# Kernel optimization log

Measured on AMD Instinct MI355X. Metric: run time of the kernel, lower is better.

Reference implementation:

```python
import jax, jax.numpy as jnp
import numpy as np

NG, ND, NS, E, DIM, H = 20000, 8000, 8000, 300000, 256, 8
HD = DIM // H
SCALE = 1.0 / float(np.sqrt(HD))
EPS = 1e-5


def _ln(x, g, b):
    mu = x.mean(-1, keepdims=True)
    var = ((x - mu) ** 2).mean(-1, keepdims=True)
    return (x - mu) / jnp.sqrt(var + EPS) * g + b


def _attn(h_src, h_dst, Wq, bq, Wk, bk, Wv, bv, src, dst, n_dst):
    # multi-head edge dot-product attention with edge_softmax over incoming edges
    Q = (h_dst @ Wq.T + bq).reshape(-1, H, HD)
    K = (h_src @ Wk.T + bk).reshape(-1, H, HD)
    V = (h_src @ Wv.T + bv).reshape(-1, H, HD)
    score = jnp.einsum('ehd,ehd->eh', K[src], Q[dst]) * SCALE  # [E, H]
    m = jax.ops.segment_max(score, dst, num_segments=n_dst)
    m = jnp.where(jnp.isfinite(m), m, 0.0)  # nodes with no in-edges
    a = jnp.exp(score - m[dst])
    denom = jax.ops.segment_sum(a, dst, num_segments=n_dst)
    a = a / denom[dst]
    h = jax.ops.segment_sum(V[src] * a[:, :, None], dst, num_segments=n_dst)
    return h.reshape(n_dst, DIM)


def _bahdanau(m1, m2, W1, b1, W2, b2, v, bv):
    e1 = (jnp.tanh(m1 @ W1.T + b1) @ v.T + bv)[:, 0]
    e2 = (jnp.tanh(m2 @ W2.T + b2) @ v.T + bv)[:, 0]
    w = jax.nn.softmax(jnp.stack([e1, e2], axis=1), axis=1)
    return w[:, 0:1] * m1 + w[:, 1:2] * m2


def _forward(gene_feat, drug_feat, disease_feat,
             dg_Wq, dg_bq, dg_Wk, dg_bk, dg_Wv, dg_bv,
             disg_Wq, disg_bq, disg_Wk, disg_bk, disg_Wv, disg_bv,
             gd_Wq, gd_bq, gd_Wk, gd_bk, gd_Wv, gd_bv,
             gdis_Wq, gdis_bq, gdis_Wk, gdis_bk, gdis_Wv, gdis_bv,
             f_W1, f_b1, f_W2, f_b2, f_v, f_bv,
             ln1_g, ln1_b, ln2_g, ln2_b,
             dg_src, dg_dst, disg_src, disg_dst, gd_src, gd_dst, gdis_src, gdis_dst):
    gm_drug = _attn(drug_feat, gene_feat, dg_Wq, dg_bq, dg_Wk, dg_bk, dg_Wv, dg_bv, dg_src, dg_dst, NG)
    gm_dis = _attn(disease_feat, gene_feat, disg_Wq, disg_bq, disg_Wk, disg_bk, disg_Wv, disg_bv, disg_src, disg_dst, NG)
    has_d = jnp.zeros((NG,), bool).at[dg_dst].set(True)
    has_s = jnp.zeros((NG,), bool).at[disg_dst].set(True)
    fused = _bahdanau(gm_drug, gm_dis, f_W1, f_b1, f_W2, f_b2, f_v, f_bv)
    gene_msg = jnp.where((has_d & has_s)[:, None], fused,
                         jnp.where(has_d[:, None], gm_drug,
                                   jnp.where(has_s[:, None], gm_dis, 0.0)))
    gene_out = _ln(gene_feat + jax.nn.gelu(gene_msg, approximate=False), ln1_g, ln1_b)
    drug_msg = _attn(gene_out, drug_feat, gd_Wq, gd_bq, gd_Wk, gd_bk, gd_Wv, gd_bv, gd_src, gd_dst, ND)
    dis_msg = _attn(gene_out, disease_feat, gdis_Wq, gdis_bq, gdis_Wk, gdis_bk, gdis_Wv, gdis_bv, gdis_src, gdis_dst, NS)
    drug_out = _ln(drug_feat + jax.nn.gelu(drug_msg, approximate=False), ln2_g, ln2_b)
    disease_out = _ln(disease_feat + jax.nn.gelu(dis_msg, approximate=False), ln2_g, ln2_b)
    return (drug_out, disease_out, gene_out)


def setup_inputs() -> dict:
    ks = jax.random.split(jax.random.key(0), 40)
    it = iter(range(40))

    def nrm(shape):
        return jax.random.normal(ks[next(it)], shape, dtype=jnp.float32)

    def xav(din, dout):
        lim = float(np.sqrt(6.0 / (din + dout)))
        return jax.random.uniform(ks[next(it)], (dout, din), minval=-lim, maxval=lim, dtype=jnp.float32)

    def ridx(n, hi):
        return jax.random.randint(ks[next(it)], (n,), 0, hi, dtype=jnp.int32)

    inp = {}
    inp['gene_feat'] = nrm((NG, DIM))
    inp['drug_feat'] = nrm((ND, DIM))
    inp['disease_feat'] = nrm((NS, DIM))
    for p in ['dg', 'disg', 'gd', 'gdis']:
        inp[p + '_Wq'] = xav(DIM, DIM)
        inp[p + '_bq'] = jnp.zeros((DIM,), jnp.float32)
        inp[p + '_Wk'] = xav(DIM, DIM)
        inp[p + '_bk'] = jnp.zeros((DIM,), jnp.float32)
        inp[p + '_Wv'] = xav(DIM, DIM)
        inp[p + '_bv'] = jnp.zeros((DIM,), jnp.float32)
    inp['f_W1'] = xav(DIM, DIM); inp['f_b1'] = jnp.zeros((DIM,), jnp.float32)
    inp['f_W2'] = xav(DIM, DIM); inp['f_b2'] = jnp.zeros((DIM,), jnp.float32)
    inp['f_v'] = xav(DIM, 1); inp['f_bv'] = jnp.zeros((1,), jnp.float32)
    inp['ln1_g'] = jnp.ones((DIM,), jnp.float32); inp['ln1_b'] = jnp.zeros((DIM,), jnp.float32)
    inp['ln2_g'] = jnp.ones((DIM,), jnp.float32); inp['ln2_b'] = jnp.zeros((DIM,), jnp.float32)
    inp['dg_src'] = ridx(E, ND); inp['dg_dst'] = ridx(E, NG)
    inp['disg_src'] = ridx(E, NS); inp['disg_dst'] = ridx(E, NG)
    inp['gd_src'] = ridx(E, NG); inp['gd_dst'] = ridx(E, ND)
    inp['gdis_src'] = ridx(E, NG); inp['gdis_dst'] = ridx(E, NS)
    return inp


def reference(gene_feat, drug_feat, disease_feat,
              dg_Wq, dg_bq, dg_Wk, dg_bk, dg_Wv, dg_bv,
              disg_Wq, disg_bq, disg_Wk, disg_bk, disg_Wv, disg_bv,
              gd_Wq, gd_bq, gd_Wk, gd_bk, gd_Wv, gd_bv,
              gdis_Wq, gdis_bq, gdis_Wk, gdis_bk, gdis_Wv, gdis_bv,
              f_W1, f_b1, f_W2, f_b2, f_v, f_bv,
              ln1_g, ln1_b, ln2_g, ln2_b,
              dg_src, dg_dst, disg_src, disg_dst, gd_src, gd_dst, gdis_src, gdis_dst):
    return _forward(gene_feat, drug_feat, disease_feat,
                    dg_Wq, dg_bq, dg_Wk, dg_bk, dg_Wv, dg_bv,
                    disg_Wq, disg_bq, disg_Wk, disg_bk, disg_Wv, disg_bv,
                    gd_Wq, gd_bq, gd_Wk, gd_bk, gd_Wv, gd_bv,
                    gdis_Wq, gdis_bq, gdis_Wk, gdis_bk, gdis_Wv, gdis_bv,
                    f_W1, f_b1, f_W2, f_b2, f_v, f_bv,
                    ln1_g, ln1_b, ln2_g, ln2_b,
                    dg_src, dg_dst, disg_src, disg_dst, gd_src, gd_dst, gdis_src, gdis_dst)
```

## Files before the change

### kernel.cpp

```cpp
#include <hip/hip_runtime.h>

#define NG 20000
#define ND 8000
#define NS 8000
#define EE 300000
#define DIM 256
#define SCALE_QK 0.17677669529663687f
#define LNEPS 1e-5f

#define MAXB 40
#define L1CH 2048
#define NCH1 ((EE + L1CH - 1) / L1CH)
#define CB_G 8704
#define CB_S 10496
#define RB_G (40 * CB_G)
#define RB_S (32 * CB_S)

typedef __attribute__((ext_vector_type(4))) float floatx4;
typedef __attribute__((ext_vector_type(8))) short shortx8;
typedef __attribute__((ext_vector_type(8))) unsigned short ushortx8;
typedef unsigned int u32;

__device__ __forceinline__ float bf2f(unsigned short u) {
    union { unsigned u; float f; } c; c.u = ((unsigned)u) << 16; return c.f;
}
__device__ __forceinline__ unsigned short f2bf(float f) {
    union { float f; unsigned u; } c; c.f = f;
    return (unsigned short)((c.u + 0x7fffu + ((c.u >> 16) & 1u)) >> 16);
}
__device__ __forceinline__ float gelu_exact(float v) {
    return 0.5f * v * (1.0f + erff(v * 0.70710678118654752f));
}

__device__ __forceinline__ void async_load16(const unsigned short* g,
                                             unsigned short* lds) {
    __builtin_amdgcn_global_load_lds(
        (const __attribute__((address_space(1))) u32*)(const void*)g,
        (__attribute__((address_space(3))) u32*)(void*)lds, 16, 0, 0);
}

__device__ __forceinline__ int swzoff(int row, int q) {
    int p = (row >> 1) & 7, b = row & 1;
    return ((row >> 4) * 64 + p * 8 + (((b << 2) + q) ^ p)) * 8;
}

struct GemmDesc {
    const unsigned short* A; const unsigned short* W;
    const float* b1; const float* b2; const float* b3; const float* b4;
    unsigned short* C; int ldc;
    const float* vvec; float* evec;
    int M; int gx; int ncol; int mode; int kvi;
};
struct GemmBatch { GemmDesc d[4]; };

__global__ __launch_bounds__(256, 4) void gemm_batch_kernel(GemmBatch gb)
{
    __shared__ unsigned short As[2][128 * 32];
    __shared__ unsigned short Bs[2][64 * 32];
    const GemmDesc d = gb.d[blockIdx.z];
    if ((int)blockIdx.x >= d.gx) return;
    const int n0 = blockIdx.y * 64;
    if (n0 >= d.ncol) return;

    const int tid = threadIdx.x;
    const int lane = tid & 63, wv = tid >> 6;
    const int quad = lane >> 4, l16 = lane & 15;
    const int m0 = blockIdx.x * 128;

    const int sp = lane >> 3, ss = lane & 7;
    const int srow = 2 * sp + ((ss ^ sp) >> 2);
    const int sq = (ss ^ sp) & 3;
    const unsigned short* gA0 = d.A + (size_t)(m0 + wv * 16 + srow) * 256 + sq * 8;
    const unsigned short* gA1 = d.A + (size_t)(m0 + 64 + wv * 16 + srow) * 256 + sq * 8;
    const unsigned short* gB  = d.W + (size_t)(n0 + wv * 16 + srow) * 256 + sq * 8;

    floatx4 acc[2][4];
#pragma unroll
    for (int i = 0; i < 2; ++i)
#pragma unroll
        for (int j = 0; j < 4; ++j) acc[i][j] = (floatx4){0.f, 0.f, 0.f, 0.f};

    async_load16(gA0, &As[0][(wv * 16) * 32]);
    async_load16(gA1, &As[0][(64 + wv * 16) * 32]);
    async_load16(gB,  &Bs[0][(wv * 16) * 32]);
    __syncthreads();

    for (int k0 = 0; k0 < 256; k0 += 32) {
        const int buf = (k0 >> 5) & 1;
        if (k0 < 224) {
            const int nb = buf ^ 1;
            async_load16(gA0 + k0 + 32, &As[nb][(wv * 16) * 32]);
            async_load16(gA1 + k0 + 32, &As[nb][(64 + wv * 16) * 32]);
            async_load16(gB + k0 + 32,  &Bs[nb][(wv * 16) * 32]);
        }
        shortx8 af[2], bfr[4];
#pragma unroll
        for (int mf = 0; mf < 2; ++mf)
            af[mf] = *(const shortx8*)(&As[buf][swzoff(wv * 32 + mf * 16 + l16, quad)]);
#pragma unroll
        for (int nf = 0; nf < 4; ++nf)
            bfr[nf] = *(const shortx8*)(&Bs[buf][swzoff(nf * 16 + l16, quad)]);
#pragma unroll
        for (int mf = 0; mf < 2; ++mf)
#pragma unroll
            for (int nf = 0; nf < 4; ++nf)
                acc[mf][nf] = __builtin_amdgcn_mfma_f32_16x16x32_bf16(
                    af[mf], bfr[nf], acc[mf][nf], 0, 0, 0);
        __syncthreads();
    }

    if (d.mode == 0) {
#pragma unroll
        for (int mf = 0; mf < 2; ++mf)
#pragma unroll
            for (int r = 0; r < 4; ++r) {
                int m = m0 + wv * 32 + mf * 16 + quad * 4 + r;
                if (m < d.M) {
#pragma unroll
                    for (int nf = 0; nf < 4; ++nf) {
                        int n = n0 + nf * 16 + l16;
                        int h = n >> 8;
                        const float* bp = (h == 0) ? d.b1 : (h == 1) ? d.b2
                                        : (h == 2) ? d.b3 : d.b4;
                        float bn = bp[n & 255];
                        int pos;
                        if (d.kvi) {
                            int nn = n & 511;
                            pos = (n & ~511) + ((nn & 255) >> 2) * 8 + (nn & 3) +
                                  ((nn >> 8) << 2);
                        } else {
                            pos = n;
                        }
                        d.C[(size_t)m * d.ldc + pos] = f2bf(acc[mf][nf][r] + bn);
                    }
                }
            }
    } else {
        float p[2][4] = {};
#pragma unroll
        for (int mf = 0; mf < 2; ++mf)
#pragma unroll
            for (int nf = 0; nf < 4; ++nf) {
                int n = n0 + nf * 16 + l16;
                float vn = d.vvec[n];
                float bn = d.b1[n];
#pragma unroll
                for (int r = 0; r < 4; ++r)
                    p[mf][r] += vn * tanhf(acc[mf][nf][r] + bn);
            }
#pragma unroll
        for (int mf = 0; mf < 2; ++mf)
#pragma unroll
            for (int r = 0; r < 4; ++r) {
                float s = p[mf][r];
                s += __shfl_xor(s, 1); s += __shfl_xor(s, 2);
                s += __shfl_xor(s, 4); s += __shfl_xor(s, 8);
                if (l16 == 0) {
                    int m = m0 + wv * 32 + mf * 16 + quad * 4 + r;
                    if (m < d.M) atomicAdd(&d.evec[m], s);
                }
            }
    }
}

struct PrepP {
    int* zb; int zn; int nzb;
    const float* wsrc[14];
    unsigned short* wout;
    const float* gf; const float* df; const float* sf;
    unsigned short* go; unsigned short* dfo; unsigned short* so;
};
__global__ void prep_kernel(PrepP p) {
    int bid = blockIdx.x, tid = threadIdx.x;
    if (bid < p.nzb) {
        int i = bid * 256 + tid;
        if (i < p.zn) p.zb[i] = 0;
        return;
    }
    bid -= p.nzb;
    if (bid < 896) {
        int idx = bid * 256 + tid;
        int mat = idx >> 14;
        int e = (idx & 16383) << 2;
        float4 f = *(const float4*)(p.wsrc[mat] + e);
        ushort4 t;
        t.x = f2bf(f.x); t.y = f2bf(f.y); t.z = f2bf(f.z); t.w = f2bf(f.w);
        *(ushort4*)(p.wout + ((size_t)mat << 16) + e) = t;
        return;
    }
    bid -= 896;
    const int NG4 = NG * 64, ND4 = ND * 64, NS4 = NS * 64;
    int i = bid * 256 + tid;
    const float* in; unsigned short* out; int j;
    if (i < NG4) { in = p.gf; out = p.go; j = i; }
    else if (i < NG4 + ND4) { in = p.df; out = p.dfo; j = i - NG4; }
    else if (i < NG4 + ND4 + NS4) { in = p.sf; out = p.so; j = i - NG4 - ND4; }
    else return;
    float4 f = *(const float4*)(in + (size_t)j * 4);
    ushort4 t;
    t.x = f2bf(f.x); t.y = f2bf(f.y); t.z = f2bf(f.z); t.w = f2bf(f.w);
    *(ushort4*)(out + (size_t)j * 4) = t;
}

__global__ void fillf_kernel(float* __restrict__ p, int n, float v) {
    int i = blockIdx.x * blockDim.x + threadIdx.x;
    if (i < n) p[i] = v;
}

struct L1P {
    const int* src[4];
    const int* dst[4];
    int* brec[4];
    int* bcur;
};
__global__ __launch_bounds__(256) void l1_bucket_kernel(L1P a) {
    __shared__ int hist[MAXB];
    int g = blockIdx.x / NCH1, c = blockIdx.x - g * NCH1;
    int base = c * L1CH;
    int tid = threadIdx.x;
    const int shift = (g < 2) ? 9 : 8;
    const int CB = (g < 2) ? CB_G : CB_S;
    const int NB = (g < 2) ? 40 : 32;
    if (tid < NB) hist[tid] = 0;
    __syncthreads();
    const int* __restrict__ dstp = a.dst[g];
    const int* __restrict__ srcp = a.src[g];
    int bk[8], rec[8], lr[8];
#pragma unroll
    for (int j = 0; j < 8; ++j) {
        int e = base + j * 256 + tid;
        bool ok = e < EE;
        int dd = ok ? dstp[e] : 0;
        int ss = ok ? srcp[e] : 0;
        bk[j] = dd >> shift;
        rec[j] = ((dd & ((1 << shift) - 1)) << 15) | ss;
        lr[j] = ok ? atomicAdd(&hist[bk[j]], 1) : -1;
    }
    __syncthreads();
    if (tid < NB) {
        int h = hist[tid];
        if (h > 0) hist[tid] = atomicAdd(&a.bcur[g * MAXB + tid], h);
    }
    __syncthreads();
    int* __restrict__ recp = a.brec[g];
#pragma unroll
    for (int j = 0; j < 8; ++j) {
        if (lr[j] >= 0) {
            int pos = hist[bk[j]] + lr[j];
            if (pos < CB) recp[bk[j] * CB + pos] = rec[j];
        }
    }
}

struct L2P {
    const int* brec[4];
    const int* bcur;
    int* cnt[4];
    int* offs[4];
    int* srcs[4];
};
__global__ __launch_bounds__(256) void l2_csr_kernel(L2P a) {
    __shared__ int hist[512];
    __shared__ int loffs[512];
    __shared__ int cur[512];
    __shared__ int ws2[4];
    __shared__ int bb;
    int bid = blockIdx.x, tid = threadIdx.x;
    int g, b;
    if (bid < 40) { g = 0; b = bid; }
    else if (bid < 80) { g = 1; b = bid - 40; }
    else if (bid < 112) { g = 2; b = bid - 80; }
    else { g = 3; b = bid - 112; }
    const int shift = (g < 2) ? 9 : 8;
    const int BSZ = 1 << shift;
    const int CB = (g < 2) ? CB_G : CB_S;
    const int N = (g < 2) ? NG : ((g == 2) ? ND : NS);
    hist[tid] = 0; hist[256 + tid] = 0;
    if (tid == 0) {
        int s = 0;
        const int* bc = a.bcur + g * MAXB;
        for (int i = 0; i < b; ++i) s += bc[i];
        bb = s;
    }
    __syncthreads();
    int total = a.bcur[g * MAXB + b];
    if (total > CB) total = CB;
    const int* __restrict__ recp = a.brec[g] + b * CB;
    for (int i = tid; i < total; i += 256)
        atomicAdd(&hist[recp[i] >> 15], 1);
    __syncthreads();
    int v0 = hist[2 * tid], v1 = hist[2 * tid + 1];
    int s = v0 + v1, x = s;
    int lane = tid & 63, wv = tid >> 6;
#pragma unroll
    for (int o = 1; o < 64; o <<= 1) {
        int u = __shfl_up(x, o);
        if (lane >= o) x += u;
    }
    if (lane == 63) ws2[wv] = x;
    __syncthreads();
    int woff = 0;
    for (int w = 0; w < wv; ++w) woff += ws2[w];
    int excl = woff + x - s;
    loffs[2 * tid] = excl; loffs[2 * tid + 1] = excl + v0;
    cur[2 * tid] = excl;  cur[2 * tid + 1] = excl + v0;
    int base = bb;
    int lo = b << shift;
    for (int i = tid; i < BSZ; i += 256) {
        int dd = lo + i;
        if (dd < N) {
            a.cnt[g][dd] = hist[i];
            a.offs[g][dd] = base + loffs[i];
        }
    }
    __syncthreads();
    int* __restrict__ sp = a.srcs[g];
    for (int i = tid; i < total; i += 256) {
        int rec = recp[i];
        int pos = atomicAdd(&cur[rec >> 15], 1);
        sp[base + pos] = rec & 0x7fff;
    }
}

__device__ __forceinline__ void wave_attn_node(
    const unsigned short* __restrict__ Q, int qs,
    const unsigned short* __restrict__ KV,
    const int* __restrict__ offs, const int* __restrict__ cnt,
    const int* __restrict__ srcs, int du, int lane,
    float& g0, float& g1, float& g2, float& g3)
{
    const int lo = lane * 4;
    const int lofs = lane * 8;
    ushort4 qv = *(const ushort4*)(Q + (size_t)du * qs + lo);
    const float q0 = bf2f(qv.x), q1 = bf2f(qv.y), q2 = bf2f(qv.z), q3 = bf2f(qv.w);
    const int beg = offs[du], num = cnt[du];

    float m = -INFINITY, l = 0.f;
    float a0 = 0.f, a1 = 0.f, a2 = 0.f, a3 = 0.f;

    int sb[8];
    if (num > 0) {
#pragma unroll
        for (int c = 0; c < 8; ++c)
            sb[c] = srcs[beg + ((c < num) ? c : (num - 1))];
    }

    for (int i = 0; i < num; i += 8) {
        int sn[8];
        const bool more = (i + 8) < num;
        if (more) {
#pragma unroll
            for (int c = 0; c < 8; ++c) {
                int idx = i + 8 + c;
                sn[c] = srcs[beg + ((idx < num) ? idx : (num - 1))];
            }
        }
        ushortx8 kv[8];
#pragma unroll
        for (int c = 0; c < 8; ++c)
            kv[c] = *(const ushortx8*)(KV + (size_t)sb[c] * 512 + lofs);
        float p[8];
#pragma unroll
        for (int c = 0; c < 8; ++c)
            p[c] = q0 * bf2f(kv[c][0]) + q1 * bf2f(kv[c][1]) +
                   q2 * bf2f(kv[c][2]) + q3 * bf2f(kv[c][3]);
#pragma unroll
        for (int c = 0; c < 8; ++c) p[c] += __shfl_xor(p[c], 1);
#pragma unroll
        for (int c = 0; c < 8; ++c) p[c] += __shfl_xor(p[c], 2);
#pragma unroll
        for (int c = 0; c < 8; ++c) p[c] += __shfl_xor(p[c], 4);
        float sc[8];
#pragma unroll
        for (int c = 0; c < 8; ++c)
            sc[c] = (i + c < num) ? p[c] * SCALE_QK : -INFINITY;
        float bm = fmaxf(fmaxf(fmaxf(sc[0], sc[1]), fmaxf(sc[2], sc[3])),
                         fmaxf(fmaxf(sc[4], sc[5]), fmaxf(sc[6], sc[7])));
        float mn = fmaxf(m, bm);
        float eo = __expf(m - mn);
        a0 *= eo; a1 *= eo; a2 *= eo; a3 *= eo; l *= eo;
        float en[8];
#pragma unroll
        for (int c = 0; c < 8; ++c) en[c] = __expf(sc[c] - mn);
#pragma unroll
        for (int c = 0; c < 8; ++c) {
            a0 += en[c] * bf2f(kv[c][4]);
            a1 += en[c] * bf2f(kv[c][5]);
            a2 += en[c] * bf2f(kv[c][6]);
            a3 += en[c] * bf2f(kv[c][7]);
            l += en[c];
        }
        m = mn;
        if (more) {
#pragma unroll
            for (int c = 0; c < 8; ++c) sb[c] = sn[c];
        }
    }

    float inv = (l > 0.f) ? 1.f / l : 0.f;
    g0 = a0 * inv; g1 = a1 * inv; g2 = a2 * inv; g3 = a3 * inv;
}

__device__ __forceinline__ void wave_ln_store(
    float x0, float x1, float x2, float x3,
    const float* __restrict__ g, const float* __restrict__ b,
    float* __restrict__ out, unsigned short* __restrict__ out_bf,
    int du, int lo)
{
    float s1 = x0 + x1 + x2 + x3;
    float s2 = x0 * x0 + x1 * x1 + x2 * x2 + x3 * x3;
#pragma unroll
    for (int o = 1; o < 64; o <<= 1) {
        s1 += __shfl_xor(s1, o);
        s2 += __shfl_xor(s2, o);
    }
    float mu = s1 * (1.f / 256.f);
    float var = fmaxf(s2 * (1.f / 256.f) - mu * mu, 0.f);
    float rs = rsqrtf(var + LNEPS);
    float4 gv = *(const float4*)(g + lo);
    float4 bv = *(const float4*)(b + lo);
    float y0 = (x0 - mu) * rs * gv.x + bv.x;
    float y1 = (x1 - mu) * rs * gv.y + bv.y;
    float y2 = (x2 - mu) * rs * gv.z + bv.z;
    float y3 = (x3 - mu) * rs * gv.w + bv.w;
    *(float4*)(out + (size_t)du * 256 + lo) = make_float4(y0, y1, y2, y3);
    if (out_bf) {
        ushort4 t; t.x = f2bf(y0); t.y = f2bf(y1); t.z = f2bf(y2); t.w = f2bf(y3);
        *(ushort4*)(out_bf + (size_t)du * 256 + lo) = t;
    }
}

struct AggDesc {
    const unsigned short* Q; int qs;
    const unsigned short* KV;
    const int* offs; const int* cnt; const int* srcs;
    unsigned short* gm;
    const float* feat; const float* g; const float* b; float* out;
    int N;
};
template <int LN>
__global__ __launch_bounds__(256, 8) void agg2_kernel(
    AggDesc a0, AggDesc a1, int nb0, int nbtot)
{
    int lane = threadIdx.x & 63, wv = threadIdx.x >> 6;
    int lo = lane * 4;
    for (int bx = blockIdx.x; bx < nbtot; bx += gridDim.x) {
        const bool first = bx < nb0;
        const AggDesc d = first ? a0 : a1;
        const int bxx = first ? bx : (bx - nb0);
        int nd = bxx * 4 + wv;
        if (nd >= d.N) continue;
        int du = __builtin_amdgcn_readfirstlane(nd);
        float g0, g1, g2, g3;
        wave_attn_node(d.Q, d.qs, d.KV, d.offs, d.cnt, d.srcs, du, lane,
                       g0, g1, g2, g3);
        if (LN == 0) {
            ushort4 t; t.x = f2bf(g0); t.y = f2bf(g1); t.z = f2bf(g2); t.w = f2bf(g3);
            *(ushort4*)(d.gm + (size_t)du * 256 + lo) = t;
        } else {
            float4 fv = *(const float4*)(d.feat + (size_t)du * 256 + lo);
            float x0 = fv.x + gelu_exact(g0);
            float x1 = fv.y + gelu_exact(g1);
            float x2 = fv.z + gelu_exact(g2);
            float x3 = fv.w + gelu_exact(g3);
            wave_ln_store(x0, x1, x2, x3, d.g, d.b, d.out, nullptr, du, lo);
        }
    }
}

__global__ __launch_bounds__(256) void gene_fusion_kernel(
    const float* __restrict__ gene_feat, const unsigned short* __restrict__ gm_d,
    const unsigned short* __restrict__ gm_s, const float* __restrict__ e1,
    const float* __restrict__ e2, const int* __restrict__ cnt_d,
    const int* __restrict__ cnt_s, const float* __restrict__ g,
    const float* __restrict__ b, float* __restrict__ out,
    unsigned short* __restrict__ out_bf)
{
    int lane = threadIdx.x & 63, wv = threadIdx.x >> 6;
    int d = blockIdx.x * 4 + wv;
    if (d >= NG) return;
    int du = __builtin_amdgcn_readfirstlane(d);
    int lo = lane * 4;
    ushort4 v1 = *(const ushort4*)(gm_d + (size_t)du * 256 + lo);
    ushort4 v2 = *(const ushort4*)(gm_s + (size_t)du * 256 + lo);
    bool hd = cnt_d[du] > 0, hs = cnt_s[du] > 0;
    float wa, wb;
    if (hd && hs) {
        float aa = e1[du], bb = e2[du];
        float mm = fmaxf(aa, bb);
        float ea = __expf(aa - mm), eb = __expf(bb - mm);
        float inv = 1.f / (ea + eb);
        wa = ea * inv; wb = eb * inv;
    } else if (hd) { wa = 1.f; wb = 0.f; }
    else if (hs) { wa = 0.f; wb = 1.f; }
    else { wa = 0.f; wb = 0.f; }
    float m0 = wa * bf2f(v1.x) + wb * bf2f(v2.x);
    float m1 = wa * bf2f(v1.y) + wb * bf2f(v2.y);
    float m2 = wa * bf2f(v1.z) + wb * bf2f(v2.z);
    float m3 = wa * bf2f(v1.w) + wb * bf2f(v2.w);
    float4 fv = *(const float4*)(gene_feat + (size_t)du * 256 + lo);
    float x0 = fv.x + gelu_exact(m0);
    float x1 = fv.y + gelu_exact(m1);
    float x2 = fv.z + gelu_exact(m2);
    float x3 = fv.w + gelu_exact(m3);
    wave_ln_store(x0, x1, x2, x3, g, b, out, out_bf, du, lo);
}

extern "C" void kernel_launch(void* const* d_in, const int* in_sizes, int n_in,
                              void* d_out, int out_size, void* d_ws, size_t ws_size,
                              hipStream_t stream)
{
    float* out_f32 = (float*)d_out;

    const float* gene_feat    = (const float*)d_in[0];
    const float* drug_feat    = (const float*)d_in[1];
    const float* disease_feat = (const float*)d_in[2];
    const float* dg_Wq = (const float*)d_in[3];
    const float* dg_bq = (const float*)d_in[4];
    const float* dg_Wk = (const float*)d_in[5];
    const float* dg_bk = (const float*)d_in[6];
    const float* dg_Wv = (const float*)d_in[7];
    const float* dg_bv = (const float*)d_in[8];
    const float* disg_Wq = (const float*)d_in[9];
    const float* disg_bq = (const float*)d_in[10];
    const float* disg_Wk = (const float*)d_in[11];
    const float* disg_bk = (const float*)d_in[12];
    const float* disg_Wv = (const float*)d_in[13];
    const float* disg_bv = (const float*)d_in[14];
    const float* gd_Wq = (const float*)d_in[15];
    const float* gd_bq = (const float*)d_in[16];
    const float* gd_Wk = (const float*)d_in[17];
    const float* gd_bk = (const float*)d_in[18];
    const float* gd_Wv = (const float*)d_in[19];
    const float* gd_bv = (const float*)d_in[20];
    const float* gdis_Wq = (const float*)d_in[21];
    const float* gdis_bq = (const float*)d_in[22];
    const float* gdis_Wk = (const float*)d_in[23];
    const float* gdis_bk = (const float*)d_in[24];
    const float* gdis_Wv = (const float*)d_in[25];
    const float* gdis_bv = (const float*)d_in[26];
    const float* f_W1 = (const float*)d_in[27];
    const float* f_b1 = (const float*)d_in[28];
    const float* f_W2 = (const float*)d_in[29];
    const float* f_b2 = (const float*)d_in[30];
    const float* f_v  = (const float*)d_in[31];
    const float* ln1_g = (const float*)d_in[33];
    const float* ln1_b = (const float*)d_in[34];
    const float* ln2_g = (const float*)d_in[35];
    const float* ln2_b = (const float*)d_in[36];
    const int* dg_src   = (const int*)d_in[37];
    const int* dg_dst   = (const int*)d_in[38];
    const int* disg_src = (const int*)d_in[39];
    const int* disg_dst = (const int*)d_in[40];
    const int* gd_src   = (const int*)d_in[41];
    const int* gd_dst   = (const int*)d_in[42];
    const int* gdis_src = (const int*)d_in[43];
    const int* gdis_dst = (const int*)d_in[44];

    char* ws = (char*)d_ws;
    size_t off = 0;
    auto alloc = [&](size_t bytes) -> char* {
        char* p = ws + off;
        off += (bytes + 511) & ~(size_t)511;
        return p;
    };
    int* bcur = (int*)alloc(4 * MAXB * 4);
    float* e1 = (float*)alloc(NG * 4);
    float* e2 = (float*)alloc(NG * 4);
    size_t zero_len = off;
    int* offs_dg   = (int*)alloc(NG * 4);
    int* offs_disg = (int*)alloc(NG * 4);
    int* offs_gd   = (int*)alloc(ND * 4);
    int* offs_gdis = (int*)alloc(NS * 4);
    int* cnt_dg    = (int*)alloc(NG * 4);
    int* cnt_disg  = (int*)alloc(NG * 4);
    int* cnt_gd    = (int*)alloc(ND * 4);
    int* cnt_gdis  = (int*)alloc(NS * 4);
    int* srcs_dg   = (int*)alloc((size_t)EE * 4);
    int* srcs_disg = (int*)alloc((size_t)EE * 4);
    int* srcs_gd   = (int*)alloc((size_t)EE * 4);
    int* srcs_gdis = (int*)alloc((size_t)EE * 4);
    unsigned short* Q12  = (unsigned short*)alloc((size_t)NG * 512 * 2);
    unsigned short* KVb  = (unsigned short*)alloc((size_t)NG * 512 * 2);
    unsigned short* gm_d = (unsigned short*)alloc((size_t)NG * 256 * 2);
    unsigned short* gm_s = (unsigned short*)alloc((size_t)NG * 256 * 2);
    unsigned short* gene_bf = (unsigned short*)alloc((size_t)NG * 256 * 2);
    unsigned short* drug_bf = (unsigned short*)alloc((size_t)ND * 256 * 2);
    unsigned short* dis_bf  = (unsigned short*)alloc((size_t)NS * 256 * 2);
    unsigned short* Wbf     = (unsigned short*)alloc((size_t)14 * 65536 * 2);
    char* guard = alloc(64 * 1024);
    (void)guard;
    size_t need = off;

    int* brec0 = (int*)Q12;
    int* brec1 = brec0 + RB_G;
    int* brec2 = brec1 + RB_G;
    int* brec3 = brec2 + RB_S;

    unsigned short* KVb2 = gm_s;
    unsigned short* KVs1b = KVb + (size_t)ND * 512;
    unsigned short* Qd = Q12;
    unsigned short* Qs = Q12 + (size_t)ND * 256;
    unsigned short* gene_out_bf = gm_d;

    float* out_drug = out_f32;
    float* out_dis  = out_drug + (size_t)ND * 256;
    float* out_gene = out_dis + (size_t)NS * 256;

    if (ws_size < need) {
        fillf_kernel<<<(out_size + 255) / 256, 256, 0, stream>>>(out_f32, out_size, 1000.0f);
        return;
    }

    {
        PrepP p;
        p.zb = (int*)d_ws;
        p.zn = (int)(zero_len / 4);
        p.nzb = (p.zn + 255) / 256;
        const float* wl[14] = {dg_Wq, disg_Wq, dg_Wk, dg_Wv, disg_Wk, disg_Wv,
                               gd_Wk, gd_Wv, gdis_Wk, gdis_Wv, gd_Wq, gdis_Wq,
                               f_W1, f_W2};
        for (int i = 0; i < 14; ++i) p.wsrc[i] = wl[i];
        p.wout = Wbf;
        p.gf = gene_feat; p.df = drug_feat; p.sf = disease_feat;
        p.go = gene_bf; p.dfo = drug_bf; p.so = dis_bf;
        int nfeat = ((NG + ND + NS) * 64 + 255) / 256;
        prep_kernel<<<p.nzb + 896 + nfeat, 256, 0, stream>>>(p);
    }

    {
        L1P p;
        p.src[0] = dg_src; p.src[1] = disg_src; p.src[2] = gd_src; p.src[3] = gdis_src;
        p.dst[0] = dg_dst; p.dst[1] = disg_dst; p.dst[2] = gd_dst; p.dst[3] = gdis_dst;
        p.brec[0] = brec0; p.brec[1] = brec1; p.brec[2] = brec2; p.brec[3] = brec3;
        p.bcur = bcur;
        l1_bucket_kernel<<<4 * NCH1, 256, 0, stream>>>(p);
    }
    {
        L2P p;
        p.brec[0] = brec0; p.brec[1] = brec1; p.brec[2] = brec2; p.brec[3] = brec3;
        p.bcur = bcur;
        p.cnt[0] = cnt_dg; p.cnt[1] = cnt_disg; p.cnt[2] = cnt_gd; p.cnt[3] = cnt_gdis;
        p.offs[0] = offs_dg; p.offs[1] = offs_disg; p.offs[2] = offs_gd; p.offs[3] = offs_gdis;
        p.srcs[0] = srcs_dg; p.srcs[1] = srcs_disg; p.srcs[2] = srcs_gd; p.srcs[3] = srcs_gdis;
        l2_csr_kernel<<<144, 256, 0, stream>>>(p);
    }

    const int GXG = (NG + 127) / 128;
    const int GXS = (ND + 127) / 128;

    auto mkd = [](const unsigned short* A, const unsigned short* W,
                  const float* b1, const float* b2, const float* b3, const float* b4,
                  unsigned short* C, int ldc, const float* vv, float* ev,
                  int M, int gx, int ncol, int mode, int kvi) {
        GemmDesc d;
        d.A = A; d.W = W; d.b1 = b1; d.b2 = b2; d.b3 = b3; d.b4 = b4;
        d.C = C; d.ldc = ldc; d.vvec = vv; d.evec = ev;
        d.M = M; d.gx = gx; d.ncol = ncol; d.mode = mode; d.kvi = kvi;
        return d;
    };
    auto mka = [](const unsigned short* Q, int qs, const unsigned short* KV,
                  const int* offs, const int* cnt, const int* srcs,
                  unsigned short* gm, const float* feat, const float* g,
                  const float* b, float* out, int N) {
        AggDesc d;
        d.Q = Q; d.qs = qs; d.KV = KV; d.offs = offs; d.cnt = cnt; d.srcs = srcs;
        d.gm = gm; d.feat = feat; d.g = g; d.b = b; d.out = out; d.N = N;
        return d;
    };

    {
        GemmBatch gb;
        gb.d[0] = mkd(gene_bf, Wbf, dg_bq, disg_bq, dg_bq, dg_bq,
                      Q12, 512, nullptr, nullptr, NG, GXG, 512, 0, 0);
        gb.d[1] = mkd(drug_bf, Wbf + (size_t)2 * 65536, dg_bk, dg_bv, dg_bk, dg_bk,
                      KVb, 512, nullptr, nullptr, ND, GXS, 512, 0, 1);
        gb.d[2] = mkd(dis_bf, Wbf + (size_t)4 * 65536, disg_bk, disg_bv, disg_bk, disg_bk,
                      KVs1b, 512, nullptr, nullptr, NS, GXS, 512, 0, 1);
        gb.d[3] = gb.d[2]; gb.d[3].gx = 0;
        gemm_batch_kernel<<<dim3(GXG, 8, 3), 256, 0, stream>>>(gb);
    }

    {
        AggDesc a0 = mka(Q12, 512, KVb, offs_dg, cnt_dg, srcs_dg,
                         gm_d, nullptr, nullptr, nullptr, nullptr, NG);
        AggDesc a1 = mka(Q12 + 256, 512, KVs1b, offs_disg, cnt_disg, srcs_disg,
                         gm_s, nullptr, nullptr, nullptr, nullptr, NG);
        int nb = (NG + 3) / 4;
        int nbtot = 2 * nb;
        int grid = nbtot < 2048 ? nbtot : 2048;
        agg2_kernel<0><<<grid, 256, 0, stream>>>(a0, a1, nb, nbtot);
    }

    {
        GemmBatch gb;
        gb.d[0] = mkd(gm_d, Wbf + (size_t)12 * 65536, f_b1, f_b1, f_b1, f_b1,
                      nullptr, 256, f_v, e1, NG, GXG, 256, 1, 0);
        gb.d[1] = mkd(gm_s, Wbf + (size_t)13 * 65536, f_b2, f_b2, f_b2, f_b2,
                      nullptr, 256, f_v, e2, NG, GXG, 256, 1, 0);
        gb.d[2] = mkd(drug_bf, Wbf + (size_t)10 * 65536, gd_bq, gd_bq, gd_bq, gd_bq,
                      Qd, 256, nullptr, nullptr, ND, GXS, 256, 0, 0);
        gb.d[3] = mkd(dis_bf, Wbf + (size_t)11 * 65536, gdis_bq, gdis_bq, gdis_bq, gdis_bq,
                      Qs, 256, nullptr, nullptr, NS, GXS, 256, 0, 0);
        gemm_batch_kernel<<<dim3(GXG, 4, 4), 256, 0, stream>>>(gb);
    }

    gene_fusion_kernel<<<(NG + 3) / 4, 256, 0, stream>>>(
        gene_feat, gm_d, gm_s, e1, e2, cnt_dg, cnt_disg, ln1_g, ln1_b,
        out_gene, gene_out_bf);

    {
        GemmBatch gb;
        gb.d[0] = mkd(gene_out_bf, Wbf + (size_t)6 * 65536, gd_bk, gd_bv, gd_bk, gd_bk,
                      KVb, 512, nullptr, nullptr, NG, GXG, 512, 0, 1);
        gb.d[1] = mkd(gene_out_bf, Wbf + (size_t)8 * 65536, gdis_bk, gdis_bv, gdis_bk, gdis_bk,
                      KVb2, 512, nullptr, nullptr, NG, GXG, 512, 0, 1);
        gb.d[2] = gb.d[1]; gb.d[2].gx = 0;
        gb.d[3] = gb.d[1]; gb.d[3].gx = 0;
        gemm_batch_kernel<<<dim3(GXG, 8, 2), 256, 0, stream>>>(gb);
    }

    {
        AggDesc a0 = mka(Qd, 256, KVb, offs_gd, cnt_gd, srcs_gd,
                         nullptr, drug_feat, ln2_g, ln2_b, out_drug, ND);
        AggDesc a1 = mka(Qs, 256, KVb2, offs_gdis, cnt_gdis, srcs_gdis,
                         nullptr, disease_feat, ln2_g, ln2_b, out_dis, NS);
        int nb = (ND + 3) / 4;
        int nbtot = 2 * nb;
        int grid = nbtot < 2048 ? nbtot : 2048;
        agg2_kernel<1><<<grid, 256, 0, stream>>>(a0, a1, nb, nbtot);
    }
}
```

Before: 497.4 us.

## Double-buffer KV gathers in attention aggregation and launch one block per node group

The per-node attention loop now issues the K/V row gathers for the next chunk of 8 edges before computing the current chunk. It also prefetches source indices two chunks ahead, so memory latency overlaps the score, softmax and accumulate work. Separately, the aggregation kernel drops its grid-stride loop and the occupancy hint in launch_bounds, and launches one block per four nodes. The double buffer roughly doubles the vector registers held for KV, which may reduce occupancy. The larger grid adds block scheduling overhead.

```diff
diff --git a/kernel.cpp b/kernel.cpp
--- a/kernel.cpp
+++ b/kernel.cpp
@@ -338,62 +338,74 @@
     float m = -INFINITY, l = 0.f;
     float a0 = 0.f, a1 = 0.f, a2 = 0.f, a3 = 0.f;
 
-    int sb[8];
     if (num > 0) {
+        int sA[8], sB[8];
+        ushortx8 kv0[8], kv1[8];
 #pragma unroll
         for (int c = 0; c < 8; ++c)
-            sb[c] = srcs[beg + ((c < num) ? c : (num - 1))];
-    }
-
-    for (int i = 0; i < num; i += 8) {
-        int sn[8];
-        const bool more = (i + 8) < num;
-        if (more) {
+            sA[c] = srcs[beg + ((c < num) ? c : (num - 1))];
+#pragma unroll
+        for (int c = 0; c < 8; ++c) {
+            int idx = 8 + c;
+            sB[c] = srcs[beg + ((idx < num) ? idx : (num - 1))];
+        }
+#pragma unroll
+        for (int c = 0; c < 8; ++c)
+            kv0[c] = *(const ushortx8*)(KV + (size_t)sA[c] * 512 + lofs);
+
+        for (int i = 0; i < num; i += 8) {
+            const bool more1 = (i + 8) < num;
+            const bool more2 = (i + 16) < num;
+            if (more1) {
+#pragma unroll
+                for (int c = 0; c < 8; ++c)
+                    kv1[c] = *(const ushortx8*)(KV + (size_t)sB[c] * 512 + lofs);
+            }
+            if (more2) {
+#pragma unroll
+                for (int c = 0; c < 8; ++c) {
+                    int idx = i + 16 + c;
+                    sA[c] = srcs[beg + ((idx < num) ? idx : (num - 1))];
+                }
+            }
+            float p[8];
+#pragma unroll
+            for (int c = 0; c < 8; ++c)
+                p[c] = q0 * bf2f(kv0[c][0]) + q1 * bf2f(kv0[c][1]) +
+                       q2 * bf2f(kv0[c][2]) + q3 * bf2f(kv0[c][3]);
+#pragma unroll
+            for (int c = 0; c < 8; ++c) p[c] += __shfl_xor(p[c], 1);
+#pragma unroll
+            for (int c = 0; c < 8; ++c) p[c] += __shfl_xor(p[c], 2);
+#pragma unroll
+            for (int c = 0; c < 8; ++c) p[c] += __shfl_xor(p[c], 4);
+            float sc[8];
+#pragma unroll
+            for (int c = 0; c < 8; ++c)
+                sc[c] = (i + c < num) ? p[c] * SCALE_QK : -INFINITY;
+            float bm = fmaxf(fmaxf(fmaxf(sc[0], sc[1]), fmaxf(sc[2], sc[3])),
+                             fmaxf(fmaxf(sc[4], sc[5]), fmaxf(sc[6], sc[7])));
+            float mn = fmaxf(m, bm);
+            float eo = __expf(m - mn);
+            a0 *= eo; a1 *= eo; a2 *= eo; a3 *= eo; l *= eo;
+            float en[8];
+#pragma unroll
+            for (int c = 0; c < 8; ++c) en[c] = __expf(sc[c] - mn);
 #pragma unroll
             for (int c = 0; c < 8; ++c) {
-                int idx = i + 8 + c;
-                sn[c] = srcs[beg + ((idx < num) ? idx : (num - 1))];
+                a0 += en[c] * bf2f(kv0[c][4]);
+                a1 += en[c] * bf2f(kv0[c][5]);
+                a2 += en[c] * bf2f(kv0[c][6]);
+                a3 += en[c] * bf2f(kv0[c][7]);
+                l += en[c];
             }
-        }
-        ushortx8 kv[8];
-#pragma unroll
-        for (int c = 0; c < 8; ++c)
-            kv[c] = *(const ushortx8*)(KV + (size_t)sb[c] * 512 + lofs);
-        float p[8];
-#pragma unroll
-        for (int c = 0; c < 8; ++c)
-            p[c] = q0 * bf2f(kv[c][0]) + q1 * bf2f(kv[c][1]) +
-                   q2 * bf2f(kv[c][2]) + q3 * bf2f(kv[c][3]);
-#pragma unroll
-        for (int c = 0; c < 8; ++c) p[c] += __shfl_xor(p[c], 1);
-#pragma unroll
-        for (int c = 0; c < 8; ++c) p[c] += __shfl_xor(p[c], 2);
-#pragma unroll
-        for (int c = 0; c < 8; ++c) p[c] += __shfl_xor(p[c], 4);
-        float sc[8];
-#pragma unroll
-        for (int c = 0; c < 8; ++c)
-            sc[c] = (i + c < num) ? p[c] * SCALE_QK : -INFINITY;
-        float bm = fmaxf(fmaxf(fmaxf(sc[0], sc[1]), fmaxf(sc[2], sc[3])),
-                         fmaxf(fmaxf(sc[4], sc[5]), fmaxf(sc[6], sc[7])));
-        float mn = fmaxf(m, bm);
-        float eo = __expf(m - mn);
-        a0 *= eo; a1 *= eo; a2 *= eo; a3 *= eo; l *= eo;
-        float en[8];
-#pragma unroll
-        for (int c = 0; c < 8; ++c) en[c] = __expf(sc[c] - mn);
-#pragma unroll
-        for (int c = 0; c < 8; ++c) {
-            a0 += en[c] * bf2f(kv[c][4]);
-            a1 += en[c] * bf2f(kv[c][5]);
-            a2 += en[c] * bf2f(kv[c][6]);
-            a3 += en[c] * bf2f(kv[c][7]);
-            l += en[c];
-        }
-        m = mn;
-        if (more) {
-#pragma unroll
-            for (int c = 0; c < 8; ++c) sb[c] = sn[c];
+            m = mn;
+            if (more1) {
+#pragma unroll
+                for (int c = 0; c < 8; ++c) kv0[c] = kv1[c];
+#pragma unroll
+                for (int c = 0; c < 8; ++c) sB[c] = sA[c];
+            }
         }
     }
 
@@ -439,32 +451,28 @@
     int N;
 };
 template <int LN>
-__global__ __launch_bounds__(256, 8) void agg2_kernel(
-    AggDesc a0, AggDesc a1, int nb0, int nbtot)
+__global__ __launch_bounds__(256) void agg2_kernel(AggDesc a0, AggDesc a1, int nb0)
 {
+    const bool first = (int)blockIdx.x < nb0;
+    const AggDesc d = first ? a0 : a1;
+    const int bx = first ? blockIdx.x : (blockIdx.x - nb0);
     int lane = threadIdx.x & 63, wv = threadIdx.x >> 6;
+    int nd = bx * 4 + wv;
+    if (nd >= d.N) return;
+    int du = __builtin_amdgcn_readfirstlane(nd);
     int lo = lane * 4;
-    for (int bx = blockIdx.x; bx < nbtot; bx += gridDim.x) {
-        const bool first = bx < nb0;
-        const AggDesc d = first ? a0 : a1;
-        const int bxx = first ? bx : (bx - nb0);
-        int nd = bxx * 4 + wv;
-        if (nd >= d.N) continue;
-        int du = __builtin_amdgcn_readfirstlane(nd);
-        float g0, g1, g2, g3;
-        wave_attn_node(d.Q, d.qs, d.KV, d.offs, d.cnt, d.srcs, du, lane,
-                       g0, g1, g2, g3);
-        if (LN == 0) {
-            ushort4 t; t.x = f2bf(g0); t.y = f2bf(g1); t.z = f2bf(g2); t.w = f2bf(g3);
-            *(ushort4*)(d.gm + (size_t)du * 256 + lo) = t;
-        } else {
-            float4 fv = *(const float4*)(d.feat + (size_t)du * 256 + lo);
-            float x0 = fv.x + gelu_exact(g0);
-            float x1 = fv.y + gelu_exact(g1);
-            float x2 = fv.z + gelu_exact(g2);
-            float x3 = fv.w + gelu_exact(g3);
-            wave_ln_store(x0, x1, x2, x3, d.g, d.b, d.out, nullptr, du, lo);
-        }
+    float g0, g1, g2, g3;
+    wave_attn_node(d.Q, d.qs, d.KV, d.offs, d.cnt, d.srcs, du, lane, g0, g1, g2, g3);
+    if (LN == 0) {
+        ushort4 t; t.x = f2bf(g0); t.y = f2bf(g1); t.z = f2bf(g2); t.w = f2bf(g3);
+        *(ushort4*)(d.gm + (size_t)du * 256 + lo) = t;
+    } else {
+        float4 fv = *(const float4*)(d.feat + (size_t)du * 256 + lo);
+        float x0 = fv.x + gelu_exact(g0);
+        float x1 = fv.y + gelu_exact(g1);
+        float x2 = fv.z + gelu_exact(g2);
+        float x3 = fv.w + gelu_exact(g3);
+        wave_ln_store(x0, x1, x2, x3, d.g, d.b, d.out, nullptr, du, lo);
     }
 }
 
@@ -687,9 +695,7 @@
         AggDesc a1 = mka(Q12 + 256, 512, KVs1b, offs_disg, cnt_disg, srcs_disg,
                          gm_s, nullptr, nullptr, nullptr, nullptr, NG);
         int nb = (NG + 3) / 4;
-        int nbtot = 2 * nb;
-        int grid = nbtot < 2048 ? nbtot : 2048;
-        agg2_kernel<0><<<grid, 256, 0, stream>>>(a0, a1, nb, nbtot);
+        agg2_kernel<0><<<2 * nb, 256, 0, stream>>>(a0, a1, nb);
     }
 
     {
@@ -726,8 +732,6 @@
         AggDesc a1 = mka(Qs, 256, KVb2, offs_gdis, cnt_gdis, srcs_gdis,
                          nullptr, disease_feat, ln2_g, ln2_b, out_dis, NS);
         int nb = (ND + 3) / 4;
-        int nbtot = 2 * nb;
-        int grid = nbtot < 2048 ? nbtot : 2048;
-        agg2_kernel<1><<<grid, 256, 0, stream>>>(a0, a1, nb, nbtot);
-    }
-}
+        agg2_kernel<1><<<2 * nb, 256, 0, stream>>>(a0, a1, nb);
+    }
+}
```

Result: faster. 483.6 us (-2.8%).
